# Optimization experiments

Measured on AMD Instinct MI355X. Metric: run time of the kernel, lower is better.

## Reference

```python
import jax, jax.numpy as jnp
import numpy as np

NUM_LAYERS = 32
NUM_SLOTS = 128
HIDDEN = 4096
T_WRITE = 128   # == NUM_SLOTS so slot_ids form a permutation (deterministic scatter)
T_READ = 8192
EMA_ALPHA = 0.1


def setup_inputs() -> dict:
    key = jax.random.key(0)
    ks = jax.random.split(key, 4)
    values = jax.random.normal(ks[0], (T_WRITE, HIDDEN), jnp.float32)
    queries = jax.random.normal(ks[1], (T_READ, HIDDEN), jnp.float32)
    memory = jax.random.normal(ks[2], (NUM_LAYERS, NUM_SLOTS, HIDDEN), jnp.float32) * 0.02
    gate_w = jax.random.normal(ks[3], (NUM_LAYERS, HIDDEN), jnp.float32) * (1.0 / np.sqrt(HIDDEN))
    gate_b = jnp.zeros((NUM_LAYERS,), jnp.float32)
    return {
        "values": values,
        "queries": queries,
        "memory": memory,
        "gate_w": gate_w,
        "gate_b": gate_b,
        "layer_idx": 0,
        "k": 8,
        "ptr": 0,
    }


def reference(values, queries, memory, gate_w, gate_b, layer_idx, k, ptr):
    # ---- write(): EMA scatter into one layer's slots ----
    mem_l = memory[layer_idx]                                  # [N, d]
    g = jax.nn.sigmoid(values @ gate_w[layer_idx] + gate_b[layer_idx])[:, None]  # [T,1]
    T = values.shape[0]
    slot_ids = (ptr + jnp.arange(T)) % NUM_SLOTS               # [T]
    current = mem_l[slot_ids]                                  # gather [T, d]
    updated = EMA_ALPHA * g * values + (1.0 - EMA_ALPHA) * current
    mem_new = mem_l.at[slot_ids].set(updated)                  # scatter-write [N, d]

    # ---- read(): matmul -> top-k -> gather -> softmax -> weighted sum ----
    scale = 1.0 / jnp.sqrt(jnp.float32(HIDDEN))
    scores = (queries @ mem_new.T) * scale                     # [T_read, N]
    topk_scores, topk_idx = jax.lax.top_k(scores, k)           # [T_read, k]
    attn = jax.nn.softmax(topk_scores, axis=-1)                # [T_read, k]
    topk_v = mem_new[topk_idx]                                 # gather [T_read, k, d]
    out = jnp.einsum('tk,tkd->td', attn, topk_v)               # [T_read, d]
    return out
```

## Files before the change

### kernel.cpp

```cpp
#include <hip/hip_runtime.h>
#include <math.h>

#define D 4096
#define NSLOTS 128
#define TR 8192
#define EPS_TRIG 5e-5f
#define WIN 2e-5f

typedef __attribute__((ext_vector_type(8))) short bf16x8;
typedef __attribute__((ext_vector_type(4))) float f32x4;

union BV { bf16x8 v; unsigned u[4]; };

__device__ __forceinline__ unsigned short bfrne(float x) {
  unsigned u = __float_as_uint(x);
  unsigned r = u + 0x7fffu + ((u >> 16) & 1u);
  return (unsigned short)(r >> 16);
}

__device__ __forceinline__ void gload16(const void* gsrc, void* ldst) {
  __builtin_amdgcn_global_load_lds(
      (const __attribute__((address_space(1))) void*)gsrc,
      (__attribute__((address_space(3))) void*)ldst, 16, 0, 0);
}

__global__ __launch_bounds__(256) void update_mem_kernel(
    const float* __restrict__ values, const float* __restrict__ memory,
    const float* __restrict__ gate_w, const float* __restrict__ gate_b,
    const int* __restrict__ layer_idx_p, const int* __restrict__ ptr_p,
    int T_W, float* __restrict__ ws_mem,
    unsigned short* __restrict__ Mh, unsigned short* __restrict__ Mm,
    unsigned short* __restrict__ Mth, unsigned short* __restrict__ Mtm) {
  const int l = layer_idx_p[0], p = ptr_p[0], s = blockIdx.x, tid = threadIdx.x;
  int t0 = ((s - p) % NSLOTS + NSLOTS) % NSLOTS;
  const bool written = (t0 < T_W);
  const int t = written ? (t0 + ((T_W - 1 - t0) / NSLOTS) * NSLOTS) : 0;
  const float* mrow = memory + ((size_t)l * NSLOTS + s) * D;
  const float* vrow = values + (size_t)t * D;

  float acoef = 0.f, bcoef = 1.0f;
  if (written) {
    const float* gw = gate_w + (size_t)l * D;
    double acc = 0.0;
    for (int j = tid; j < D; j += 256)
      acc += (double)vrow[j] * (double)gw[j];
    for (int off = 32; off; off >>= 1) acc += __shfl_down(acc, off, 64);
    __shared__ double wsum[4];
    if ((tid & 63) == 0) wsum[tid >> 6] = acc;
    __syncthreads();
    double dot = wsum[0] + wsum[1] + wsum[2] + wsum[3];
    float x = (float)dot + gate_b[l];
    float g = 1.0f / (1.0f + expf(-x));
    acoef = 0.1f * g; bcoef = 0.9f;
  }

  for (int j4 = tid; j4 < D / 4; j4 += 256) {
    float4 mv = ((const float4*)mrow)[j4];
    float4 vv = make_float4(0.f, 0.f, 0.f, 0.f);
    if (written) vv = ((const float4*)vrow)[j4];
    float ov[4];
    ov[0] = acoef * vv.x + bcoef * mv.x;
    ov[1] = acoef * vv.y + bcoef * mv.y;
    ov[2] = acoef * vv.z + bcoef * mv.z;
    ov[3] = acoef * vv.w + bcoef * mv.w;
    ((float4*)(ws_mem + (size_t)s * D))[j4] =
        make_float4(ov[0], ov[1], ov[2], ov[3]);
    unsigned short h[4], md[4];
#pragma unroll
    for (int e = 0; e < 4; ++e) {
      h[e] = bfrne(ov[e]);
      float f = __uint_as_float((unsigned)h[e] << 16);
      md[e] = bfrne(ov[e] - f);
    }
    uint2 hp = make_uint2((unsigned)h[0] | ((unsigned)h[1] << 16),
                          (unsigned)h[2] | ((unsigned)h[3] << 16));
    uint2 mp = make_uint2((unsigned)md[0] | ((unsigned)md[1] << 16),
                          (unsigned)md[2] | ((unsigned)md[3] << 16));
    ((uint2*)Mh)[(size_t)s * (D / 4) + j4] = hp;
    ((uint2*)Mm)[(size_t)s * (D / 4) + j4] = mp;
#pragma unroll
    for (int e = 0; e < 4; ++e) {
      Mth[(size_t)(j4 * 4 + e) * NSLOTS + s] = h[e];
      Mtm[(size_t)(j4 * 4 + e) * NSLOTS + s] = md[e];
    }
  }
}

__global__ __launch_bounds__(256) void scores_kernel(
    const float* __restrict__ queries, const unsigned short* __restrict__ Mh,
    const unsigned short* __restrict__ Mm, float* __restrict__ part) {
  __shared__ float4 QsV[2][8 * 128];
  __shared__ bf16x8 MhV[2][4 * 128];
  __shared__ bf16x8 MmV[2][4 * 128];

  const int tid = threadIdx.x, lane = tid & 63, w = tid >> 6;
  const int fr = lane & 15, fo = lane >> 4;
  const int qt = blockIdx.x >> 3, kq = blockIdx.x & 7;
  const int qbase = qt * 128;
  const int kbase = kq * 512;

  const float* qsrc[4];
#pragma unroll
  for (int i = 0; i < 4; ++i) {
    int idx = w * 256 + i * 64 + lane;
    int u = idx >> 7, row = idx & 127;
    qsrc[i] = queries + (size_t)(qbase + row) * D + kbase + u * 4;
  }
  const unsigned short *mhsrc[2], *mmsrc[2];
#pragma unroll
  for (int i = 0; i < 2; ++i) {
    int idx = w * 128 + i * 64 + lane;
    int u = idx >> 7, slot = idx & 127;
    mhsrc[i] = Mh + (size_t)slot * D + kbase + u * 8;
    mmsrc[i] = Mm + (size_t)slot * D + kbase + u * 8;
  }

  f32x4 acc[2][8];
#pragma unroll
  for (int rg = 0; rg < 2; ++rg)
#pragma unroll
    for (int cg = 0; cg < 8; ++cg) acc[rg][cg] = (f32x4){0.f, 0.f, 0.f, 0.f};

  const int rowA = w * 32 + fr;

#define SC_STAGE(B, S) do {                                                  \
    const int k0_ = (S) * 32;                                                \
    _Pragma("unroll")                                                        \
    for (int i = 0; i < 4; ++i)                                              \
      gload16(qsrc[i] + k0_, &QsV[B][w * 256 + i * 64]);                     \
    _Pragma("unroll")                                                        \
    for (int i = 0; i < 2; ++i) {                                            \
      gload16(mhsrc[i] + k0_, &MhV[B][w * 128 + i * 64]);                    \
      gload16(mmsrc[i] + k0_, &MmV[B][w * 128 + i * 64]);                    \
    }                                                                        \
  } while (0)

#define SC_COMPUTE(B) do {                                                   \
    _Pragma("unroll")                                                        \
    for (int rg = 0; rg < 2; ++rg) {                                         \
      const int row = rowA + rg * 16;                                        \
      float4 a0 = QsV[B][(fo * 2 + 0) * 128 + row];                          \
      float4 a1 = QsV[B][(fo * 2 + 1) * 128 + row];                          \
      float qf[8] = {a0.x, a0.y, a0.z, a0.w, a1.x, a1.y, a1.z, a1.w};        \
      BV ah, am;                                                             \
      _Pragma("unroll")                                                      \
      for (int i = 0; i < 4; ++i) {                                          \
        unsigned u0 = __float_as_uint(qf[2 * i]);                            \
        unsigned u1 = __float_as_uint(qf[2 * i + 1]);                        \
        ah.u[i] = (u0 >> 16) | (u1 & 0xffff0000u);                           \
        float f0 = __uint_as_float(u0 & 0xffff0000u);                        \
        float f1 = __uint_as_float(u1 & 0xffff0000u);                        \
        unsigned d0 = __float_as_uint(qf[2 * i] - f0);                       \
        unsigned d1 = __float_as_uint(qf[2 * i + 1] - f1);                   \
        am.u[i] = (d0 >> 16) | (d1 & 0xffff0000u);                           \
      }                                                                      \
      _Pragma("unroll")                                                      \
      for (int cg = 0; cg < 8; ++cg) {                                       \
        const int slot = cg * 16 + fr;                                       \
        bf16x8 bh = MhV[B][fo * 128 + slot];                                 \
        bf16x8 bm = MmV[B][fo * 128 + slot];                                 \
        acc[rg][cg] = __builtin_amdgcn_mfma_f32_16x16x32_bf16(am.v, bh, acc[rg][cg], 0, 0, 0); \
        acc[rg][cg] = __builtin_amdgcn_mfma_f32_16x16x32_bf16(ah.v, bm, acc[rg][cg], 0, 0, 0); \
        acc[rg][cg] = __builtin_amdgcn_mfma_f32_16x16x32_bf16(ah.v, bh, acc[rg][cg], 0, 0, 0); \
      }                                                                      \
    }                                                                        \
  } while (0)

  SC_STAGE(0, 0);
  __syncthreads();

  for (int t = 0; t < 8; ++t) {
    SC_STAGE(1, 2 * t + 1);
    SC_COMPUTE(0);
    __syncthreads();
    if (t < 7) SC_STAGE(0, 2 * t + 2);
    SC_COMPUTE(1);
    __syncthreads();
  }
#undef SC_STAGE
#undef SC_COMPUTE

  float* op = part + ((size_t)kq * TR + qbase) * NSLOTS;
#pragma unroll
  for (int rg = 0; rg < 2; ++rg)
#pragma unroll
    for (int cg = 0; cg < 8; ++cg)
#pragma unroll
      for (int r = 0; r < 4; ++r)
        op[(size_t)(w * 32 + rg * 16 + fo * 4 + r) * NSLOTS + cg * 16 + fr] =
            acc[rg][cg][r];
}

__device__ __forceinline__ unsigned mapf(float f) {
  unsigned u = __float_as_uint(f);
  return (u & 0x80000000u) ? ~u : (u | 0x80000000u);
}
__device__ __forceinline__ float unmapf(unsigned u) {
  return __uint_as_float((u & 0x80000000u) ? (u & 0x7fffffffu) : ~u);
}

__device__ __forceinline__ void wave_select(
    float va, float vb, int l, int k, int iters,
    float &m, float &sum, bool &sela, bool &selb, float &vkm1, float &vkk) {
  m = 0.f; sum = 0.f; sela = false; selb = false; vkm1 = 0.f; vkk = -3.4e38f;
  for (int it = 0; it < iters; ++it) {
    unsigned long long ka =
        ((unsigned long long)mapf(va) << 32) | (unsigned)(127 - l);
    unsigned long long kb =
        ((unsigned long long)mapf(vb) << 32) | (unsigned)(63 - l);
    unsigned long long key = ka > kb ? ka : kb;
#pragma unroll
    for (int off = 32; off; off >>= 1) {
      unsigned long long o = __shfl_xor(key, off, 64);
      if (o > key) key = o;
    }
    int idx = 127 - (int)(unsigned)(key & 0xffffffffULL);
    float val = unmapf((unsigned)(key >> 32));
    if (it == 0) m = val;
    if (it < k) sum += expf(val - m);
    if (it == k - 1) vkm1 = val;
    if (it == k) vkk = val;
    if (idx == l) { sela = sela || (it < k); va = -INFINITY; }
    if (idx == l + 64) { selb = selb || (it < k); vb = -INFINITY; }
  }
}

__device__ __forceinline__ float rescore_slot(const float* __restrict__ qrow,
                                              const float* __restrict__ mrow,
                                              int l) {
  double acc = 0.0;
#pragma unroll 4
  for (int c = 0; c < 16; ++c) {
    int j = c * 256 + l * 4;
    float4 qv = *(const float4*)(qrow + j);
    float4 mv = *(const float4*)(mrow + j);
    acc += (double)qv.x * (double)mv.x;
    acc += (double)qv.y * (double)mv.y;
    acc += (double)qv.z * (double)mv.z;
    acc += (double)qv.w * (double)mv.w;
  }
#pragma unroll
  for (int off = 32; off; off >>= 1) acc += __shfl_xor(acc, off, 64);
  return (float)(acc * 0.015625);
}

__global__ __launch_bounds__(256) void topk_kernel(
    const float* __restrict__ part, const float* __restrict__ ws_mem,
    const float* __restrict__ queries, const int* __restrict__ k_p,
    unsigned short* __restrict__ Ah, unsigned short* __restrict__ Am) {
  const int w = threadIdx.x >> 6, l = threadIdx.x & 63;
  const int row = blockIdx.x * 4 + w;
  int k = k_p[0];
  if (k < 1) k = 1;
  if (k > NSLOTS) k = NSLOTS;
  const int ksel = (k < NSLOTS) ? k + 1 : k;

  float origa = 0.f, origb = 0.f;
#pragma unroll
  for (int kq = 0; kq < 8; ++kq) {
    origa += part[((size_t)kq * TR + row) * NSLOTS + l];
    origb += part[((size_t)kq * TR + row) * NSLOTS + 64 + l];
  }
  origa *= 0.015625f;
  origb *= 0.015625f;

  float m, sum, vkm1, vkk;
  bool sela, selb;
  wave_select(origa, origb, l, k, ksel, m, sum, sela, selb, vkm1, vkk);

  if (ksel > k && (vkm1 - vkk) < EPS_TRIG) {
    const float* qrow = queries + (size_t)row * D;
    float lo = vkk - WIN, hi = vkm1 + WIN;
    unsigned long long ba = __ballot(origa >= lo && origa <= hi);
    unsigned long long bb = __ballot(origb >= lo && origb <= hi);
    while (ba) {
      int s = __ffsll(ba) - 1; ba &= ba - 1;
      float ex = rescore_slot(qrow, ws_mem + (size_t)s * D, l);
      if (l == s) origa = ex;
    }
    while (bb) {
      int s = __ffsll(bb) - 1; bb &= bb - 1;
      float ex = rescore_slot(qrow, ws_mem + (size_t)(s + 64) * D, l);
      if (l == s) origb = ex;
    }
    wave_select(origa, origb, l, k, k, m, sum, sela, selb, vkm1, vkk);
  }

  const float inv = 1.0f / sum;
  float wa = sela ? expf(origa - m) * inv : 0.f;
  float wb = selb ? expf(origb - m) * inv : 0.f;

  unsigned short ha = bfrne(wa);
  unsigned short ma = bfrne(wa - __uint_as_float((unsigned)ha << 16));
  unsigned short hb = bfrne(wb);
  unsigned short mb = bfrne(wb - __uint_as_float((unsigned)hb << 16));
  Ah[(size_t)row * NSLOTS + l] = ha;
  Am[(size_t)row * NSLOTS + l] = ma;
  Ah[(size_t)row * NSLOTS + 64 + l] = hb;
  Am[(size_t)row * NSLOTS + 64 + l] = mb;
}

__global__ __launch_bounds__(256) void gather_kernel(
    const unsigned short* __restrict__ Ah, const unsigned short* __restrict__ Am,
    const unsigned short* __restrict__ Mth, const unsigned short* __restrict__ Mtm,
    float* __restrict__ out) {
  __shared__ char lds[65536];
  const int tid = threadIdx.x, lane = tid & 63, w = tid >> 6;
  const int fr = lane & 15, fo = lane >> 4;
  const int rowblk = blockIdx.x >> 6, colblk = blockIdx.x & 63;
  const int r0 = rowblk * 64, c0 = colblk * 64;

  const unsigned short* srcbase =
      (w == 0) ? Ah + (size_t)r0 * NSLOTS :
      (w == 1) ? Am + (size_t)r0 * NSLOTS :
      (w == 2) ? Mth + (size_t)c0 * NSLOTS :
                 Mtm + (size_t)c0 * NSLOTS;
#pragma unroll
  for (int i = 0; i < 16; ++i) {
    int dl = i * 64 + lane;
    int row = dl >> 4, u = dl & 15;
    int su = u ^ (row & 7);
    gload16(srcbase + (size_t)row * NSLOTS + su * 8,
            lds + w * 16384 + i * 1024);
  }
  __syncthreads();

  const int rw = w >> 1, cw = w & 1;
  f32x4 acc[2][2];
#pragma unroll
  for (int rg = 0; rg < 2; ++rg)
#pragma unroll
    for (int cg = 0; cg < 2; ++cg) acc[rg][cg] = (f32x4){0.f, 0.f, 0.f, 0.f};

#pragma unroll
  for (int c = 0; c < 4; ++c) {
    bf16x8 ah_[2], am_[2], bh_[2], bm_[2];
#pragma unroll
    for (int rg = 0; rg < 2; ++rg) {
      int row = rw * 32 + rg * 16 + fr;
      int off = row * 256 + ((c * 64 + fo * 16) ^ ((row & 7) << 4));
      ah_[rg] = *(const bf16x8*)(lds + off);
      am_[rg] = *(const bf16x8*)(lds + 16384 + off);
    }
#pragma unroll
    for (int cg = 0; cg < 2; ++cg) {
      int col = cw * 32 + cg * 16 + fr;
      int off = col * 256 + ((c * 64 + fo * 16) ^ ((col & 7) << 4));
      bh_[cg] = *(const bf16x8*)(lds + 32768 + off);
      bm_[cg] = *(const bf16x8*)(lds + 49152 + off);
    }
#pragma unroll
    for (int rg = 0; rg < 2; ++rg)
#pragma unroll
      for (int cg = 0; cg < 2; ++cg) {
        acc[rg][cg] = __builtin_amdgcn_mfma_f32_16x16x32_bf16(am_[rg], bh_[cg], acc[rg][cg], 0, 0, 0);
        acc[rg][cg] = __builtin_amdgcn_mfma_f32_16x16x32_bf16(ah_[rg], bm_[cg], acc[rg][cg], 0, 0, 0);
        acc[rg][cg] = __builtin_amdgcn_mfma_f32_16x16x32_bf16(ah_[rg], bh_[cg], acc[rg][cg], 0, 0, 0);
      }
  }
  __syncthreads();

  float* O = (float*)lds;
#pragma unroll
  for (int rg = 0; rg < 2; ++rg)
#pragma unroll
    for (int cg = 0; cg < 2; ++cg)
#pragma unroll
      for (int r = 0; r < 4; ++r)
        O[(rw * 32 + rg * 16 + fo * 4 + r) * 132 + cw * 32 + cg * 16 + fr] =
            acc[rg][cg][r];
  __syncthreads();

#pragma unroll
  for (int i = 0; i < 4; ++i) {
    int idx = tid + i * 256;
    int row = idx >> 4, c4 = idx & 15;
    float4 v = *(const float4*)(O + row * 132 + c4 * 4);
    *(float4*)(out + (size_t)(r0 + row) * D + c0 + c4 * 4) = v;
  }
}

extern "C" void kernel_launch(void* const* d_in, const int* in_sizes, int n_in,
                              void* d_out, int out_size, void* d_ws, size_t ws_size,
                              hipStream_t stream) {
  const float* values  = (const float*)d_in[0];
  const float* queries = (const float*)d_in[1];
  const float* memory  = (const float*)d_in[2];
  const float* gate_w  = (const float*)d_in[3];
  const float* gate_b  = (const float*)d_in[4];
  const int* layer_idx = (const int*)d_in[5];
  const int* k_p       = (const int*)d_in[6];
  const int* ptr_p     = (const int*)d_in[7];

  const int T_W = in_sizes[0] / D;
  const int T_R = in_sizes[1] / D;

  float* ws_mem = (float*)d_ws;
  float* part   = ws_mem + (size_t)NSLOTS * D;
  unsigned short* Mh  = (unsigned short*)(part + (size_t)8 * TR * NSLOTS);
  unsigned short* Mm  = Mh  + (size_t)NSLOTS * D;
  unsigned short* Mth = Mm  + (size_t)NSLOTS * D;
  unsigned short* Mtm = Mth + (size_t)NSLOTS * D;
  unsigned short* Ah  = Mtm + (size_t)NSLOTS * D;
  unsigned short* Am  = Ah  + (size_t)T_R * NSLOTS;

  update_mem_kernel<<<NSLOTS, 256, 0, stream>>>(
      values, memory, gate_w, gate_b, layer_idx, ptr_p, T_W,
      ws_mem, Mh, Mm, Mth, Mtm);
  scores_kernel<<<(T_R / 128) * 8, 256, 0, stream>>>(queries, Mh, Mm, part);
  topk_kernel<<<T_R / 4, 256, 0, stream>>>(part, ws_mem, queries, k_p, Ah, Am);
  gather_kernel<<<(T_R / 64) * (D / 64), 256, 0, stream>>>(Ah, Am, Mth, Mtm,
                                                           (float*)d_out);
}
```

Measured before the change: 165.1 us.

## Pre-swizzle memory into MFMA fragment layout and read B operands directly from global

The update kernel now writes the bf16 hi/lo memory copies in a fragment-ordered layout, so each lane in the scores kernel can load its B operands with one 16-byte global load, with no trip through LDS. The scores kernel stages only queries in LDS, using an XOR swizzle to avoid bank conflicts. The loop becomes a single-buffered-step ping-pong over 16 k-steps. This cuts LDS traffic and shared-memory footprint, but B loads now hit L2/global inside the compute loop with less latency hiding.

```diff
diff --git a/kernel.cpp b/kernel.cpp
--- a/kernel.cpp
+++ b/kernel.cpp
@@ -4,6 +4,8 @@
 #define D 4096
 #define NSLOTS 128
 #define TR 8192
+#define NKQ 8
+#define KCH 512
 #define EPS_TRIG 5e-5f
 #define WIN 2e-5f
 
@@ -29,7 +31,7 @@
     const float* __restrict__ gate_w, const float* __restrict__ gate_b,
     const int* __restrict__ layer_idx_p, const int* __restrict__ ptr_p,
     int T_W, float* __restrict__ ws_mem,
-    unsigned short* __restrict__ Mh, unsigned short* __restrict__ Mm,
+    unsigned short* __restrict__ MFh, unsigned short* __restrict__ MFm,
     unsigned short* __restrict__ Mth, unsigned short* __restrict__ Mtm) {
   const int l = layer_idx_p[0], p = ptr_p[0], s = blockIdx.x, tid = threadIdx.x;
   int t0 = ((s - p) % NSLOTS + NSLOTS) % NSLOTS;
@@ -54,66 +56,80 @@
     acoef = 0.1f * g; bcoef = 0.9f;
   }
 
-  for (int j4 = tid; j4 < D / 4; j4 += 256) {
-    float4 mv = ((const float4*)mrow)[j4];
-    float4 vv = make_float4(0.f, 0.f, 0.f, 0.f);
-    if (written) vv = ((const float4*)vrow)[j4];
-    float ov[4];
-    ov[0] = acoef * vv.x + bcoef * mv.x;
-    ov[1] = acoef * vv.y + bcoef * mv.y;
-    ov[2] = acoef * vv.z + bcoef * mv.z;
-    ov[3] = acoef * vv.w + bcoef * mv.w;
-    ((float4*)(ws_mem + (size_t)s * D))[j4] =
+  const int sg = s >> 4, fr = s & 15;
+  for (int j8 = tid; j8 < D / 8; j8 += 256) {
+    float4 mv0 = ((const float4*)mrow)[j8 * 2];
+    float4 mv1 = ((const float4*)mrow)[j8 * 2 + 1];
+    float4 vv0 = make_float4(0.f, 0.f, 0.f, 0.f), vv1 = vv0;
+    if (written) {
+      vv0 = ((const float4*)vrow)[j8 * 2];
+      vv1 = ((const float4*)vrow)[j8 * 2 + 1];
+    }
+    float ov[8];
+    ov[0] = acoef * vv0.x + bcoef * mv0.x;
+    ov[1] = acoef * vv0.y + bcoef * mv0.y;
+    ov[2] = acoef * vv0.z + bcoef * mv0.z;
+    ov[3] = acoef * vv0.w + bcoef * mv0.w;
+    ov[4] = acoef * vv1.x + bcoef * mv1.x;
+    ov[5] = acoef * vv1.y + bcoef * mv1.y;
+    ov[6] = acoef * vv1.z + bcoef * mv1.z;
+    ov[7] = acoef * vv1.w + bcoef * mv1.w;
+    ((float4*)(ws_mem + (size_t)s * D))[j8 * 2] =
         make_float4(ov[0], ov[1], ov[2], ov[3]);
-    unsigned short h[4], md[4];
-#pragma unroll
-    for (int e = 0; e < 4; ++e) {
+    ((float4*)(ws_mem + (size_t)s * D))[j8 * 2 + 1] =
+        make_float4(ov[4], ov[5], ov[6], ov[7]);
+
+    unsigned short h[8], md[8];
+#pragma unroll
+    for (int e = 0; e < 8; ++e) {
       h[e] = bfrne(ov[e]);
       float f = __uint_as_float((unsigned)h[e] << 16);
       md[e] = bfrne(ov[e] - f);
     }
-    uint2 hp = make_uint2((unsigned)h[0] | ((unsigned)h[1] << 16),
-                          (unsigned)h[2] | ((unsigned)h[3] << 16));
-    uint2 mp = make_uint2((unsigned)md[0] | ((unsigned)md[1] << 16),
-                          (unsigned)md[2] | ((unsigned)md[3] << 16));
-    ((uint2*)Mh)[(size_t)s * (D / 4) + j4] = hp;
-    ((uint2*)Mm)[(size_t)s * (D / 4) + j4] = mp;
-#pragma unroll
-    for (int e = 0; e < 4; ++e) {
-      Mth[(size_t)(j4 * 4 + e) * NSLOTS + s] = h[e];
-      Mtm[(size_t)(j4 * 4 + e) * NSLOTS + s] = md[e];
+    const int ks = j8 >> 2, fo = j8 & 3;
+    const size_t unit = (size_t)ks * 512 + sg * 64 + fo * 16 + fr;
+    uint4 hp, mp;
+    hp.x = (unsigned)h[0] | ((unsigned)h[1] << 16);
+    hp.y = (unsigned)h[2] | ((unsigned)h[3] << 16);
+    hp.z = (unsigned)h[4] | ((unsigned)h[5] << 16);
+    hp.w = (unsigned)h[6] | ((unsigned)h[7] << 16);
+    mp.x = (unsigned)md[0] | ((unsigned)md[1] << 16);
+    mp.y = (unsigned)md[2] | ((unsigned)md[3] << 16);
+    mp.z = (unsigned)md[4] | ((unsigned)md[5] << 16);
+    mp.w = (unsigned)md[6] | ((unsigned)md[7] << 16);
+    ((uint4*)MFh)[unit] = hp;
+    ((uint4*)MFm)[unit] = mp;
+#pragma unroll
+    for (int e = 0; e < 8; ++e) {
+      Mth[(size_t)(j8 * 8 + e) * NSLOTS + s] = h[e];
+      Mtm[(size_t)(j8 * 8 + e) * NSLOTS + s] = md[e];
     }
   }
 }
 
 __global__ __launch_bounds__(256) void scores_kernel(
-    const float* __restrict__ queries, const unsigned short* __restrict__ Mh,
-    const unsigned short* __restrict__ Mm, float* __restrict__ part) {
-  __shared__ float4 QsV[2][8 * 128];
-  __shared__ bf16x8 MhV[2][4 * 128];
-  __shared__ bf16x8 MmV[2][4 * 128];
+    const float* __restrict__ queries, const unsigned short* __restrict__ MFh,
+    const unsigned short* __restrict__ MFm, float* __restrict__ part) {
+  __shared__ float Qs[2][4096];
 
   const int tid = threadIdx.x, lane = tid & 63, w = tid >> 6;
   const int fr = lane & 15, fo = lane >> 4;
-  const int qt = blockIdx.x >> 3, kq = blockIdx.x & 7;
+  const int qt = blockIdx.x >> 3, kq = blockIdx.x & (NKQ - 1);
   const int qbase = qt * 128;
-  const int kbase = kq * 512;
-
+  const int kbase = kq * KCH;
+
+  const int rl = lane >> 3, ul = lane & 7;
+  const int su = ul ^ rl;
   const float* qsrc[4];
 #pragma unroll
   for (int i = 0; i < 4; ++i) {
-    int idx = w * 256 + i * 64 + lane;
-    int u = idx >> 7, row = idx & 127;
-    qsrc[i] = queries + (size_t)(qbase + row) * D + kbase + u * 4;
-  }
-  const unsigned short *mhsrc[2], *mmsrc[2];
-#pragma unroll
-  for (int i = 0; i < 2; ++i) {
-    int idx = w * 128 + i * 64 + lane;
-    int u = idx >> 7, slot = idx & 127;
-    mhsrc[i] = Mh + (size_t)slot * D + kbase + u * 8;
-    mmsrc[i] = Mm + (size_t)slot * D + kbase + u * 8;
-  }
+    int g = w * 4 + i;
+    qsrc[i] = queries + (size_t)(qbase + 8 * g + rl) * D + kbase + su * 4;
+  }
+
+  const unsigned short* bh_base = MFh + (size_t)lane * 8;
+  const unsigned short* bm_base = MFm + (size_t)lane * 8;
+  const size_t kqoff = (size_t)kq * 16 * 512 * 8;
 
   f32x4 acc[2][8];
 #pragma unroll
@@ -121,26 +137,26 @@
 #pragma unroll
     for (int cg = 0; cg < 8; ++cg) acc[rg][cg] = (f32x4){0.f, 0.f, 0.f, 0.f};
 
-  const int rowA = w * 32 + fr;
-
-#define SC_STAGE(B, S) do {                                                  \
+#define STG(B, S) do {                                                       \
     const int k0_ = (S) * 32;                                                \
     _Pragma("unroll")                                                        \
     for (int i = 0; i < 4; ++i)                                              \
-      gload16(qsrc[i] + k0_, &QsV[B][w * 256 + i * 64]);                     \
+      gload16(qsrc[i] + k0_, &Qs[B][(w * 4 + i) * 256]);                     \
+  } while (0)
+
+#define CMP(B, S) do {                                                       \
+    const size_t soff = kqoff + (size_t)(S) * 512 * 8;                       \
+    bf16x8 bh_[8], bm_[8];                                                   \
     _Pragma("unroll")                                                        \
-    for (int i = 0; i < 2; ++i) {                                            \
-      gload16(mhsrc[i] + k0_, &MhV[B][w * 128 + i * 64]);                    \
-      gload16(mmsrc[i] + k0_, &MmV[B][w * 128 + i * 64]);                    \
+    for (int cg = 0; cg < 8; ++cg) {                                         \
+      bh_[cg] = *(const bf16x8*)(bh_base + soff + cg * 64 * 8);              \
+      bm_[cg] = *(const bf16x8*)(bm_base + soff + cg * 64 * 8);              \
     }                                                                        \
-  } while (0)
-
-#define SC_COMPUTE(B) do {                                                   \
     _Pragma("unroll")                                                        \
     for (int rg = 0; rg < 2; ++rg) {                                         \
-      const int row = rowA + rg * 16;                                        \
-      float4 a0 = QsV[B][(fo * 2 + 0) * 128 + row];                          \
-      float4 a1 = QsV[B][(fo * 2 + 1) * 128 + row];                          \
+      const int row = w * 32 + rg * 16 + fr;                                 \
+      float4 a0 = *(const float4*)&Qs[B][row * 32 + (((fo * 2) ^ (row & 7)) << 2)]; \
+      float4 a1 = *(const float4*)&Qs[B][row * 32 + ((((fo * 2) | 1) ^ (row & 7)) << 2)]; \
       float qf[8] = {a0.x, a0.y, a0.z, a0.w, a1.x, a1.y, a1.z, a1.w};        \
       BV ah, am;                                                             \
       _Pragma("unroll")                                                      \
@@ -156,29 +172,23 @@
       }                                                                      \
       _Pragma("unroll")                                                      \
       for (int cg = 0; cg < 8; ++cg) {                                       \
-        const int slot = cg * 16 + fr;                                       \
-        bf16x8 bh = MhV[B][fo * 128 + slot];                                 \
-        bf16x8 bm = MmV[B][fo * 128 + slot];                                 \
-        acc[rg][cg] = __builtin_amdgcn_mfma_f32_16x16x32_bf16(am.v, bh, acc[rg][cg], 0, 0, 0); \
-        acc[rg][cg] = __builtin_amdgcn_mfma_f32_16x16x32_bf16(ah.v, bm, acc[rg][cg], 0, 0, 0); \
-        acc[rg][cg] = __builtin_amdgcn_mfma_f32_16x16x32_bf16(ah.v, bh, acc[rg][cg], 0, 0, 0); \
+        acc[rg][cg] = __builtin_amdgcn_mfma_f32_16x16x32_bf16(am.v, bh_[cg], acc[rg][cg], 0, 0, 0); \
+        acc[rg][cg] = __builtin_amdgcn_mfma_f32_16x16x32_bf16(ah.v, bm_[cg], acc[rg][cg], 0, 0, 0); \
+        acc[rg][cg] = __builtin_amdgcn_mfma_f32_16x16x32_bf16(ah.v, bh_[cg], acc[rg][cg], 0, 0, 0); \
       }                                                                      \
     }                                                                        \
   } while (0)
 
-  SC_STAGE(0, 0);
+  STG(0, 0);
   __syncthreads();
-
-  for (int t = 0; t < 8; ++t) {
-    SC_STAGE(1, 2 * t + 1);
-    SC_COMPUTE(0);
+  for (int s = 0; s < 16; ++s) {
+    const int cur = s & 1;
+    if (s < 15) STG(cur ^ 1, s + 1);
+    CMP(cur, s);
     __syncthreads();
-    if (t < 7) SC_STAGE(0, 2 * t + 2);
-    SC_COMPUTE(1);
-    __syncthreads();
-  }
-#undef SC_STAGE
-#undef SC_COMPUTE
+  }
+#undef STG
+#undef CMP
 
   float* op = part + ((size_t)kq * TR + qbase) * NSLOTS;
 #pragma unroll
@@ -257,7 +267,7 @@
 
   float origa = 0.f, origb = 0.f;
 #pragma unroll
-  for (int kq = 0; kq < 8; ++kq) {
+  for (int kq = 0; kq < NKQ; ++kq) {
     origa += part[((size_t)kq * TR + row) * NSLOTS + l];
     origb += part[((size_t)kq * TR + row) * NSLOTS + 64 + l];
   }
@@ -397,17 +407,17 @@
 
   float* ws_mem = (float*)d_ws;
   float* part   = ws_mem + (size_t)NSLOTS * D;
-  unsigned short* Mh  = (unsigned short*)(part + (size_t)8 * TR * NSLOTS);
-  unsigned short* Mm  = Mh  + (size_t)NSLOTS * D;
-  unsigned short* Mth = Mm  + (size_t)NSLOTS * D;
+  unsigned short* MFh = (unsigned short*)(part + (size_t)NKQ * TR * NSLOTS);
+  unsigned short* MFm = MFh + (size_t)NSLOTS * D;
+  unsigned short* Mth = MFm + (size_t)NSLOTS * D;
   unsigned short* Mtm = Mth + (size_t)NSLOTS * D;
   unsigned short* Ah  = Mtm + (size_t)NSLOTS * D;
   unsigned short* Am  = Ah  + (size_t)T_R * NSLOTS;
 
   update_mem_kernel<<<NSLOTS, 256, 0, stream>>>(
       values, memory, gate_w, gate_b, layer_idx, ptr_p, T_W,
-      ws_mem, Mh, Mm, Mth, Mtm);
-  scores_kernel<<<(T_R / 128) * 8, 256, 0, stream>>>(queries, Mh, Mm, part);
+      ws_mem, MFh, MFm, Mth, Mtm);
+  scores_kernel<<<(T_R / 128) * NKQ, 256, 0, stream>>>(queries, MFh, MFm, part);
   topk_kernel<<<T_R / 4, 256, 0, stream>>>(part, ws_mem, queries, k_p, Ah, Am);
   gather_kernel<<<(T_R / 64) * (D / 64), 256, 0, stream>>>(Ah, Am, Mth, Mtm,
                                                            (float*)d_out);
```

Result: faster. 142.4 us (-13.8%).
